# Performance work log

Hardware: AMD Instinct MI355X
Metric: run time of the kernel (lower is better)

Reference implementation:

```python
import jax, jax.numpy as jnp
import numpy as np

B, S, C = 16, 2048, 512
E = S            # embed_dim == seq_len (RMSNorm applied on transposed seq axis)
H = 4 * E        # FFN hidden
LAMBDA_INIT = float(0.8 - 0.6 * np.exp(-0.3 * 1.0))  # layer_index = 1
SCALE = E ** (-0.25)
K = 5            # decomposition moving-average kernel


def rmsnorm(x, w, eps=1e-8):
    return x * jax.lax.rsqrt(jnp.mean(x * x, axis=-1, keepdims=True) + eps) * w


def decompose(a):
    # DLinear-style series decomposition: replicate-padded moving average along seq
    pad = (K - 1) // 2
    ap = jnp.concatenate([jnp.repeat(a[:, :1], pad, axis=1), a, jnp.repeat(a[:, -1:], pad, axis=1)], axis=1)
    n = a.shape[1]
    trend = sum(ap[:, i:i + n] for i in range(K)) / K
    return trend, a - trend


def setup_inputs() -> dict:
    key = jax.random.key(0)
    ks = jax.random.split(key, 12)
    p = lambda i, shape, s=0.02: jax.random.normal(ks[i], shape, jnp.float32) * s
    return {
        "x": jax.random.normal(ks[0], (B, S, C), jnp.float32),
        "ln_attn_w": jnp.ones((E,), jnp.float32),
        "q12_w": p(1, (E, 2 * E)), "q12_b": jnp.zeros((2 * E,), jnp.float32),
        "k12_w": p(2, (E, 2 * E)), "k12_b": jnp.zeros((2 * E,), jnp.float32),
        "v_w": p(3, (E, E)), "v_b": jnp.zeros((E,), jnp.float32),
        "lambda_q1": p(4, (E,), 0.1), "lambda_k1": p(5, (E,), 0.1),
        "lambda_q2": p(6, (E,), 0.1), "lambda_k2": p(7, (E,), 0.1),
        "norm_w": jnp.ones((E,), jnp.float32),
        "ln_ff_w": jnp.ones((E,), jnp.float32),
        "ff_w1": p(8, (E, H)), "ff_b1": jnp.zeros((H,), jnp.float32),
        "ff_w2": p(9, (H, E)), "ff_b2": jnp.zeros((E,), jnp.float32),
    }


def reference(x, ln_attn_w, q12_w, q12_b, k12_w, k12_b, v_w, v_b,
              lambda_q1, lambda_k1, lambda_q2, lambda_k2,
              norm_w, ln_ff_w, ff_w1, ff_b1, ff_w2, ff_b2):
    # pre-attention RMSNorm over the seq axis (via transpose)
    a = jnp.swapaxes(rmsnorm(jnp.swapaxes(x, -1, -2), ln_attn_w), -1, -2)  # [B,S,C]
    trend, seasonal = decompose(a)
    # project seq dim of trend/seasonal (iTransformer style: channels are tokens)
    q = jnp.swapaxes(trend, -1, -2) @ q12_w + q12_b      # [B,C,2S]
    q1, q2 = jnp.split(q, 2, axis=-1)                    # [B,C,S] each
    k = jnp.swapaxes(seasonal, -1, -2) @ k12_w + k12_b   # [B,C,2S]
    k1, k2 = jnp.split(k, 2, axis=-1)                    # [B,C,S]
    v = jnp.swapaxes(a, -1, -2) @ v_w + v_b              # [B,C,S]
    a1 = jnp.einsum('bis,bjs->bij', q1, k1) * SCALE      # [B,C,C]
    a2 = jnp.einsum('bis,bjs->bij', q2, k2) * SCALE      # [B,C,C]
    lam = jnp.exp(jnp.sum(lambda_q1 * lambda_k1)) - jnp.exp(jnp.sum(lambda_q2 * lambda_k2)) + LAMBDA_INIT
    d = jax.nn.softmax(a1, axis=-1) - lam * jax.nn.softmax(a2, axis=-1)
    attn = rmsnorm(d @ v, norm_w) * (1.0 - LAMBDA_INIT)  # [B,C,S]
    x = x + jnp.swapaxes(attn, -1, -2)
    # FFN over the seq axis
    h = rmsnorm(jnp.swapaxes(x, -1, -2), ln_ff_w)        # [B,C,S]
    ff = jax.nn.gelu(h @ ff_w1 + ff_b1, approximate=False) @ ff_w2 + ff_b2
    return x + jnp.swapaxes(ff, -1, -2)
```

## Files before the change

kernel.cpp:

```cpp
#include <hip/hip_runtime.h>
#include <hip/hip_bf16.h>

#define B_ 16
#define S_ 2048
#define C_ 512
#define H_ 8192

#define LAMBDA_INIT_F 0.3555090675909693f
#define ONE_M_LI_F    0.6444909324090307f
#define SCALE_F       0.14865088937534013f

using bf16x8 = __attribute__((ext_vector_type(8))) short;
using f32x4  = __attribute__((ext_vector_type(4))) float;

__device__ __forceinline__ float b2f(ushort u) {
  union { unsigned u; float f; } x; x.u = ((unsigned)u) << 16; return x.f;
}
__device__ __forceinline__ ushort f2b(float f) {
  union { float f; unsigned u; } x; x.f = f;
  unsigned r = x.u + 0x7fffu + ((x.u >> 16) & 1u);
  return (ushort)(r >> 16);
}

__device__ __forceinline__ void load_lds16(const void* g, void* s) {
  __builtin_amdgcn_global_load_lds((const __attribute__((address_space(1))) void*)g,
                                   (__attribute__((address_space(3))) void*)s,
                                   16, 0, 0);
}

#define WAITV8() asm volatile("s_waitcnt vmcnt(8)" ::: "memory")
#define WAITV4() asm volatile("s_waitcnt vmcnt(4)" ::: "memory")
#define WAITV0() asm volatile("s_waitcnt vmcnt(0)" ::: "memory")
#define BARM()   asm volatile("s_barrier" ::: "memory")
#define BAR()    __builtin_amdgcn_s_barrier()

template <int EPI>
__global__ __launch_bounds__(512, 1) void gemm256(
    const ushort* __restrict__ A, const ushort* __restrict__ Bt,
    ushort* __restrict__ C, const float* __restrict__ bias,
    const ushort* __restrict__ addm,
    int K, int lda, int ldb, int ldc)
{
  __shared__ ushort lds[65536];
  const int t = threadIdx.x, w = t >> 6, lane = t & 63;
  const int fr = lane & 15, khl = lane >> 4;
  const int wr = w >> 2, wc = w & 3;

  const int gx = gridDim.x, gy = gridDim.y;
  const int id = blockIdx.y * gx + blockIdx.x;
  const int xcd = id & 7, l = id >> 3;
  const int tnb = (gy == 16) ? 3 : 2;
  const int lm = l >> tnb, ln = l & ((1 << tnb) - 1);
  const int m0 = ((xcd & 3) * 8 + lm) * 256;
  const int n0 = ((xcd >> 2) * (1 << tnb) + ln) * 256;

  const int sl    = (t & 7) ^ ((t >> 3) & 7);
  const int rbase = ((t >> 3) << 1) + (sl >> 2);
  const int khs   = sl & 3;
  const size_t aoff = (size_t)(m0 + rbase) * lda + khs * 8;
  const size_t boff = (size_t)(n0 + rbase) * ldb + khs * 8;
  const size_t jstA = (size_t)128 * lda, jstB = (size_t)128 * ldb;

  int ao[8], bo[4];
#pragma unroll
  for (int m = 0; m < 8; ++m) {
    const int row = wr * 128 + m * 16 + fr, dr = row >> 1;
    const int so = (((row & 1) << 2) + khl) ^ (dr & 7);
    ao[m] = dr * 64 + so * 8;
  }
#pragma unroll
  for (int n = 0; n < 4; ++n) {
    const int row = wc * 64 + n * 16 + fr, dr = row >> 1;
    const int so = (((row & 1) << 2) + khl) ^ (dr & 7);
    bo[n] = 8192 + dr * 64 + so * 8;
  }

  f32x4 acc[8][4] = {};
  const int U = K >> 5;

#define STAGE_U(u) do { \
    const ushort* sa_ = A  + aoff + (size_t)(u) * 32; \
    const ushort* sb_ = Bt + boff + (size_t)(u) * 32; \
    ushort* da_ = &lds[((u) & 3) * 16384 + w * 512]; \
    load_lds16(sa_, da_); load_lds16(sa_ + jstA, da_ + 4096); \
    load_lds16(sb_, da_ + 8192); load_lds16(sb_ + jstB, da_ + 12288); } while (0)
#define LDFRAG(u) do { const int sb_ = ((u) & 3) * 16384; \
    _Pragma("unroll") for (int m_ = 0; m_ < 8; ++m_) af[m_] = *(const bf16x8*)&lds[sb_ + ao[m_]]; \
    _Pragma("unroll") for (int n_ = 0; n_ < 4; ++n_) bg[n_] = *(const bf16x8*)&lds[sb_ + bo[n_]]; } while (0)
#define MFMA32() do { __builtin_amdgcn_s_setprio(1); \
    _Pragma("unroll") for (int m_ = 0; m_ < 8; ++m_) \
    _Pragma("unroll") for (int n_ = 0; n_ < 4; ++n_) \
      acc[m_][n_] = __builtin_amdgcn_mfma_f32_16x16x32_bf16(af[m_], bg[n_], acc[m_][n_], 0, 0, 0); \
    __builtin_amdgcn_s_setprio(0); } while (0)

  STAGE_U(0); STAGE_U(1); STAGE_U(2);
  WAITV8(); BARM();

  bf16x8 af[8], bg[4];
#pragma unroll 4
  for (int u = 0; u <= U - 4; ++u) {
    LDFRAG(u);
    STAGE_U(u + 3);
    MFMA32();
    WAITV8();
    BARM();
  }
  {
    LDFRAG(U - 3);
    MFMA32();
    WAITV4();
    BARM();
  }
  {
    LDFRAG(U - 2);
    MFMA32();
    WAITV0();
    BARM();
  }
  {
    LDFRAG(U - 1);
    MFMA32();
  }
#undef STAGE_U
#undef LDFRAG
#undef MFMA32

  const int r0 = khl * 4;
#pragma unroll
  for (int m = 0; m < 8; ++m)
#pragma unroll
    for (int nf = 0; nf < 4; ++nf) {
      const int gr = m0 + wr * 128 + m * 16 + r0;
      const int gc = n0 + wc * 64 + nf * 16 + fr;
      const float bb = (EPI == 3) ? 0.f : bias[gc];
#pragma unroll
      for (int r = 0; r < 4; ++r) {
        const size_t idx = (size_t)(gr + r) * ldc + gc;
        float v = acc[m][nf][r];
        if constexpr (EPI == 1) v += bb;
        if constexpr (EPI == 2) { v += bb; v = 0.5f * v * (1.f + erff(v * 0.7071067811865475f)); }
        if constexpr (EPI == 4) v += bb + b2f(addm[idx]) + b2f(C[idx]);
        C[idx] = f2b(v);
      }
    }
}

template <int EPI>
__global__ __launch_bounds__(256, 2) void gemm_nt(
    const ushort* __restrict__ Aall, const ushort* __restrict__ Ball,
    void* __restrict__ Call, int K, int lda, int ldb, int ldc,
    long sA, long sB, long sC, long sA2, long sB2, float alpha,
    const float* __restrict__ bias)
{
  __shared__ ushort lA[4096];
  __shared__ ushort lB[4096];
  const int t = threadIdx.x;
  const int m0 = blockIdx.x * 128, n0 = blockIdx.y * 128;
  const int zb = blockIdx.z & 15, zh = blockIdx.z >> 4;
  const ushort* A  = Aall + (size_t)zb * sA + (size_t)zh * sA2;
  const ushort* Bt = Ball + (size_t)zb * sB + (size_t)zh * sB2;
  const int lane = t & 63;
  const int wave = t >> 6;
  const int wm = (wave >> 1) * 64, wn = (wave & 1) * 64;
  const int fr = lane & 15, kh = lane >> 4;
  f32x4 acc[4][4] = {};
  const int srow = t >> 2;
  const int scol = (t & 3) * 8;
  const size_t ar0 = (size_t)(m0 + srow) * lda + scol;
  const size_t ar1 = (size_t)(m0 + 64 + srow) * lda + scol;
  const size_t br0 = (size_t)(n0 + srow) * ldb + scol;
  const size_t br1 = (size_t)(n0 + 64 + srow) * ldb + scol;
  const int wbase = wave * 512;

  for (int k0 = 0; k0 < K; k0 += 32) {
    __syncthreads();
    load_lds16(A + ar0 + k0,  &lA[wbase]);
    load_lds16(A + ar1 + k0,  &lA[2048 + wbase]);
    load_lds16(Bt + br0 + k0, &lB[wbase]);
    load_lds16(Bt + br1 + k0, &lB[2048 + wbase]);
    __syncthreads();
    bf16x8 af[4], bg[4];
#pragma unroll
    for (int i = 0; i < 4; ++i)
      af[i] = *(const bf16x8*)&lA[(wm + i * 16 + fr) * 32 + kh * 8];
#pragma unroll
    for (int j = 0; j < 4; ++j)
      bg[j] = *(const bf16x8*)&lB[(wn + j * 16 + fr) * 32 + kh * 8];
#pragma unroll
    for (int i = 0; i < 4; ++i)
#pragma unroll
      for (int j = 0; j < 4; ++j)
        acc[i][j] = __builtin_amdgcn_mfma_f32_16x16x32_bf16(af[i], bg[j], acc[i][j], 0, 0, 0);
  }

  const int r0 = kh * 4;
  if constexpr (EPI == 0) {
    float* C = (float*)Call + (size_t)blockIdx.z * sC;
#pragma unroll
    for (int i = 0; i < 4; ++i)
#pragma unroll
      for (int j = 0; j < 4; ++j) {
        const int gr = m0 + wm + i * 16 + r0;
        const int gc = n0 + wn + j * 16 + fr;
#pragma unroll
        for (int r = 0; r < 4; ++r)
          C[(size_t)(gr + r) * ldc + gc] = acc[i][j][r] * alpha;
      }
  } else {
    ushort* C = (ushort*)Call + (size_t)blockIdx.z * sC;
#pragma unroll
    for (int i = 0; i < 4; ++i)
#pragma unroll
      for (int j = 0; j < 4; ++j) {
        const int gr = m0 + wm + i * 16 + r0;
        const int gc = n0 + wn + j * 16 + fr;
#pragma unroll
        for (int r = 0; r < 4; ++r) {
          float v = acc[i][j][r];
          if constexpr (EPI == 3) v *= alpha;
          if constexpr (EPI == 5) v += bias[gr + r];
          C[(size_t)(gr + r) * ldc + gc] = f2b(v);
        }
      }
  }
}

__device__ __forceinline__ float block_sum(float v, float* red) {
#pragma unroll
  for (int o = 32; o > 0; o >>= 1) v += __shfl_down(v, o, 64);
  __syncthreads();
  if ((threadIdx.x & 63) == 0) red[threadIdx.x >> 6] = v;
  __syncthreads();
  return red[0] + red[1] + red[2] + red[3];
}
__device__ __forceinline__ float block_max(float v, float* red) {
#pragma unroll
  for (int o = 32; o > 0; o >>= 1) v = fmaxf(v, __shfl_down(v, o, 64));
  __syncthreads();
  if ((threadIdx.x & 63) == 0) red[threadIdx.x >> 6] = v;
  __syncthreads();
  return fmaxf(fmaxf(red[0], red[1]), fmaxf(red[2], red[3]));
}

__global__ __launch_bounds__(256) void k_rms_part(const float* __restrict__ x, float* __restrict__ part) {
  const int c = blockIdx.x * 256 + threadIdx.x;
  const int sl = blockIdx.y;
  const int b = blockIdx.z;
  const float* p = x + (size_t)b * S_ * C_ + c;
  const int s0 = sl * 256;
  float s = 0.f;
  for (int i = 0; i < 256; ++i) { float v = p[(size_t)(s0 + i) * C_]; s += v * v; }
  part[((size_t)b * C_ + c) * 8 + sl] = s;
}
__global__ __launch_bounds__(256) void k_rms_fin(const float* __restrict__ part, float* __restrict__ rms1) {
  const int i = blockIdx.x * 256 + threadIdx.x;
  const float* p = part + (size_t)i * 8;
  float s = 0.f;
#pragma unroll
  for (int j = 0; j < 8; ++j) s += p[j];
  rms1[i] = rsqrtf(s * (1.f / S_) + 1e-8f);
}

__global__ __launch_bounds__(256) void k_trans_norm(const float* __restrict__ x, const float* __restrict__ rms1,
                                                    const float* __restrict__ w,
                                                    ushort* __restrict__ aT, ushort* __restrict__ xT) {
  __shared__ float tile[32][33];
  const int s0 = blockIdx.x * 32, c0 = blockIdx.y * 32, b = blockIdx.z;
  const int tx = threadIdx.x, ty = threadIdx.y;
  const float* xb = x + (size_t)b * S_ * C_;
#pragma unroll
  for (int r = 0; r < 4; ++r) {
    const int s = ty + 8 * r;
    tile[s][tx] = xb[(size_t)(s0 + s) * C_ + c0 + tx];
  }
  __syncthreads();
#pragma unroll
  for (int r = 0; r < 4; ++r) {
    const int c = ty + 8 * r;
    const float v = tile[tx][c];
    const float rm = rms1[b * C_ + c0 + c];
    const size_t o = ((size_t)b * C_ + c0 + c) * S_ + s0 + tx;
    xT[o] = f2b(v);
    aT[o] = f2b(v * rm * w[s0 + tx]);
  }
}

__global__ __launch_bounds__(256) void k_wtrans(const float* __restrict__ W, ushort* __restrict__ WT,
                                                int Kd, int Ndstride, int n_base) {
  __shared__ float tile[32][33];
  const int k0 = blockIdx.x * 32, n0 = blockIdx.y * 32;
  const int tx = threadIdx.x, ty = threadIdx.y;
#pragma unroll
  for (int r = 0; r < 4; ++r) {
    const int k = ty + 8 * r;
    tile[k][tx] = W[(size_t)(k0 + k) * Ndstride + n_base + n0 + tx];
  }
  __syncthreads();
#pragma unroll
  for (int r = 0; r < 4; ++r) {
    const int n = ty + 8 * r;
    WT[(size_t)(n0 + n) * Kd + k0 + tx] = f2b(tile[tx][n]);
  }
}

__global__ __launch_bounds__(256) void k_convert(const float* __restrict__ in, ushort* __restrict__ out) {
  const size_t i = ((size_t)blockIdx.x * 256 + threadIdx.x) * 8;
  const f32x4 v0 = *(const f32x4*)(in + i);
  const f32x4 v1 = *(const f32x4*)(in + i + 4);
  bf16x8 o;
#pragma unroll
  for (int j = 0; j < 4; ++j) { o[j] = (short)f2b(v0[j]); o[4 + j] = (short)f2b(v1[j]); }
  *(bf16x8*)(out + i) = o;
}

__global__ __launch_bounds__(256) void k_matvec(const float* __restrict__ kw, const float* __restrict__ qb,
                                                float* __restrict__ vv) {
  __shared__ float red[4];
  const int s = blockIdx.x;
  const float* row = kw + (size_t)s * 4096;
  const int t = threadIdx.x;
  float s1 = 0.f, s2 = 0.f;
  for (int i = t; i < 2048; i += 256) { s1 += row[i] * qb[i]; s2 += row[2048 + i] * qb[2048 + i]; }
  s1 = block_sum(s1, red);
  s2 = block_sum(s2, red);
  if (t == 0) { vv[s] = s1; vv[2048 + s] = s2; }
}

__global__ __launch_bounds__(256) void k_gemv(const ushort* __restrict__ seT, const float* __restrict__ vv,
                                              float* __restrict__ rvec) {
  __shared__ float red[4];
  const int r = blockIdx.x;
  const ushort* row = seT + (size_t)r * 2048;
  const int t = threadIdx.x;
  float s1 = 0.f, s2 = 0.f;
  for (int i = t; i < 2048; i += 256) {
    const float sv = b2f(row[i]);
    s1 += sv * vv[i]; s2 += sv * vv[2048 + i];
  }
  s1 = block_sum(s1, red);
  s2 = block_sum(s2, red);
  if (t == 0) { rvec[r] = SCALE_F * s1; rvec[8192 + r] = SCALE_F * s2; }
}

__device__ __forceinline__ float trend5(const ushort* p, int s) {
  float sum = 0.f;
#pragma unroll
  for (int d = -2; d <= 2; ++d) {
    int ss = s + d; ss = ss < 0 ? 0 : (ss > S_ - 1 ? S_ - 1 : ss);
    sum += b2f(p[ss]);
  }
  return sum * 0.2f;
}
__global__ __launch_bounds__(256) void k_decomp2(const ushort* __restrict__ aT,
                                                 ushort* __restrict__ trT, ushort* __restrict__ seT) {
  const size_t i = (size_t)blockIdx.x * 256 + threadIdx.x;
  const int s = (int)(i & (S_ - 1));
  const ushort* p = aT + (i - s);
  const float tr = trend5(p, s);
  trT[i] = f2b(tr);
  seT[i] = f2b(b2f(p[s]) - tr);
}

__global__ __launch_bounds__(256) void k_lambda(const float* __restrict__ lq1, const float* __restrict__ lk1,
                                                const float* __restrict__ lq2, const float* __restrict__ lk2,
                                                float* __restrict__ lam) {
  __shared__ float r1[4], r2[4];
  const int t = threadIdx.x;
  float s1 = 0.f, s2 = 0.f;
  for (int i = t; i < S_; i += 256) { s1 += lq1[i] * lk1[i]; s2 += lq2[i] * lk2[i]; }
#pragma unroll
  for (int o = 32; o > 0; o >>= 1) { s1 += __shfl_down(s1, o, 64); s2 += __shfl_down(s2, o, 64); }
  if ((t & 63) == 0) { r1[t >> 6] = s1; r2[t >> 6] = s2; }
  __syncthreads();
  if (t == 0) {
    const float a = r1[0] + r1[1] + r1[2] + r1[3];
    const float b = r2[0] + r2[1] + r2[2] + r2[3];
    *lam = expf(a) - expf(b) + LAMBDA_INIT_F;
  }
}

__global__ __launch_bounds__(256) void k_softmax(const float* __restrict__ a1, const float* __restrict__ a2,
                                                 const float* __restrict__ lamp, const float* __restrict__ rvec,
                                                 ushort* __restrict__ dm) {
  __shared__ float red[4];
  const size_t row = blockIdx.x;
  const int jb = ((int)row >> 9) << 9;
  const float* p1 = a1 + row * 512;
  const float* p2 = a2 + row * 512;
  const int t = threadIdx.x;
  const float v1a = p1[t] + rvec[jb + t],        v1b = p1[t + 256] + rvec[jb + t + 256];
  const float v2a = p2[t] + rvec[8192 + jb + t], v2b = p2[t + 256] + rvec[8192 + jb + t + 256];
  const float m1 = block_max(fmaxf(v1a, v1b), red);
  const float m2 = block_max(fmaxf(v2a, v2b), red);
  const float e1a = expf(v1a - m1), e1b = expf(v1b - m1);
  const float e2a = expf(v2a - m2), e2b = expf(v2b - m2);
  const float s1 = block_sum(e1a + e1b, red);
  const float s2 = block_sum(e2a + e2b, red);
  const float i1 = 1.f / s1, i2 = (*lamp) / s2;
  ushort* o = dm + row * 512;
  o[t]       = f2b(e1a * i1 - e2a * i2);
  o[t + 256] = f2b(e1b * i1 - e2b * i2);
}

__global__ __launch_bounds__(256) void k_postattn(const ushort* __restrict__ P, const ushort* __restrict__ xT,
                                                  const float* __restrict__ norm_w, const float* __restrict__ ln_ff_w,
                                                  ushort* __restrict__ attn, ushort* __restrict__ h) {
  __shared__ float red[4];
  const size_t row = blockIdx.x;
  const ushort* p = P + row * S_;
  const int t = threadIdx.x;
  float v[8]; float ss = 0.f;
#pragma unroll
  for (int i = 0; i < 8; ++i) { v[i] = b2f(p[t + 256 * i]); ss += v[i] * v[i]; }
  ss = block_sum(ss, red);
  const float inv = rsqrtf(ss * (1.f / S_) + 1e-8f);
  const ushort* xr = xT + row * S_;
  ushort* ar = attn + row * S_;
  float x2[8]; float ss2 = 0.f;
#pragma unroll
  for (int i = 0; i < 8; ++i) {
    const int s = t + 256 * i;
    const float at = v[i] * inv * norm_w[s] * ONE_M_LI_F;
    ar[s] = f2b(at);
    const float xx = b2f(xr[s]) + at;
    x2[i] = xx; ss2 += xx * xx;
  }
  ss2 = block_sum(ss2, red);
  const float inv2 = rsqrtf(ss2 * (1.f / S_) + 1e-8f);
  ushort* hr = h + row * S_;
#pragma unroll
  for (int i = 0; i < 8; ++i) { const int s = t + 256 * i; hr[s] = f2b(x2[i] * inv2 * ln_ff_w[s]); }
}

__global__ __launch_bounds__(256) void k_final2(const float* __restrict__ x, const ushort* __restrict__ sumT,
                                                float* __restrict__ out) {
  __shared__ float tile[32][33];
  const int s0 = blockIdx.x * 32, c0 = blockIdx.y * 32, b = blockIdx.z;
  const int tx = threadIdx.x, ty = threadIdx.y;
#pragma unroll
  for (int r = 0; r < 4; ++r) {
    const int c = ty + 8 * r;
    tile[c][tx] = b2f(sumT[((size_t)b * C_ + c0 + c) * S_ + s0 + tx]);
  }
  __syncthreads();
#pragma unroll
  for (int r = 0; r < 4; ++r) {
    const int s = ty + 8 * r;
    const size_t o = ((size_t)b * S_ + s0 + s) * C_ + c0 + tx;
    out[o] = x[o] + tile[tx][s];
  }
}

__global__ void k_probe(float* out, float v) { out[0] = v; }

extern "C" void kernel_launch(void* const* d_in, const int* in_sizes, int n_in,
                              void* d_out, int out_size, void* d_ws, size_t ws_size,
                              hipStream_t stream) {
  const float* x       = (const float*)d_in[0];
  const float* ln_attn = (const float*)d_in[1];
  const float* q12_w   = (const float*)d_in[2];
  const float* q12_b   = (const float*)d_in[3];
  const float* k12_w   = (const float*)d_in[4];
  const float* k12_b   = (const float*)d_in[5];
  const float* v_w     = (const float*)d_in[6];
  const float* v_b     = (const float*)d_in[7];
  const float* lq1     = (const float*)d_in[8];
  const float* lk1     = (const float*)d_in[9];
  const float* lq2     = (const float*)d_in[10];
  const float* lk2     = (const float*)d_in[11];
  const float* norm_w  = (const float*)d_in[12];
  const float* ln_ff   = (const float*)d_in[13];
  const float* ff_w1   = (const float*)d_in[14];
  const float* ff_b1   = (const float*)d_in[15];
  const float* ff_w2   = (const float*)d_in[16];
  const float* ff_b2   = (const float*)d_in[17];
  float* out = (float*)d_out;

  if (ws_size < 184844544ull) {
    k_probe<<<1, 1, 0, stream>>>(out, (float)(ws_size >> 20));
    return;
  }

  char* ws = (char*)d_ws;
  ushort* slotA = (ushort*)(ws + 0);
  ushort* slotB = (ushort*)(ws + 33554432);
  ushort* slotC = (ushort*)(ws + 67108864);
  ushort* slotD = (ushort*)(ws + 100663296);
  ushort* slotE = (ushort*)(ws + 134217728);
  ushort* slotF = (ushort*)(ws + 167772160);
  float*  part  = (float*) (ws + 184549376);
  float*  rms1  = (float*) (ws + 184811520);
  float*  lamp  = (float*) (ws + 184844288);

  ushort* aT   = slotA;
  ushort* k12c = slotA;
  ushort* T12s = slotA;
  ushort* hbuf = slotA;
  ushort* trT  = slotB;
  ushort* Pm   = slotB;
  ushort* ff1T = slotB;
  ushort* seT  = slotC;
  ushort* attn = slotC;
  ushort* VT   = slotD;
  ushort* ff2T = slotD;
  ushort* xT   = slotE;
  ushort* ffo  = slotE;
  ushort* wsl  = slotF;
  ushort* q12c = slotF;
  ushort* dmat = slotF;
  float*  vvb  = (float*)(ws + 167772160 + 12582912);
  float*  rvec = vvb + 4096;
  ushort* M12T = (ushort*)d_out;
  float*  scr  = (float*)((char*)d_out + 16777216);
  ushort* H1   = (ushort*)d_out;

  const dim3 blk256(256), blk512(512), blkT(32, 8);

  k_rms_part<<<dim3(2, 8, B_), blk256, 0, stream>>>(x, part);
  k_rms_fin<<<dim3(32), blk256, 0, stream>>>(part, rms1);
  k_trans_norm<<<dim3(64, 16, B_), blkT, 0, stream>>>(x, rms1, ln_attn, aT, xT);

  k_wtrans<<<dim3(64, 64), blkT, 0, stream>>>(v_w, wsl, 2048, 2048, 0);
  gemm_nt<5><<<dim3(16, 4, 16), blk256, 0, stream>>>(wsl, aT, VT, 2048, 2048, 2048, 512,
                                                     0, 1048576, 1048576, 0, 0, 1.f, v_b);

  k_decomp2<<<dim3(65536), blk256, 0, stream>>>(aT, trT, seT);
  k_lambda<<<dim3(1), blk256, 0, stream>>>(lq1, lk1, lq2, lk2, lamp);

  k_convert<<<dim3(4096), blk256, 0, stream>>>(q12_w, q12c);
  k_convert<<<dim3(4096), blk256, 0, stream>>>(k12_w, k12c);
  gemm_nt<3><<<dim3(16, 16, 2), blk256, 0, stream>>>(k12c, q12c, M12T, 2048, 4096, 4096, 2048,
                                                     2048, 2048, 4194304, 0, 0, 1.f, nullptr);

  k_matvec<<<dim3(2048), blk256, 0, stream>>>(k12_w, q12_b, vvb);
  k_gemv<<<dim3(8192), blk256, 0, stream>>>(seT, vvb, rvec);

  gemm256<3><<<dim3(32, 8), blk512, 0, stream>>>(trT, M12T, T12s, nullptr, nullptr,
                                                 2048, 2048, 2048, 2048);
  gemm_nt<0><<<dim3(4, 4, 16), blk256, 0, stream>>>(T12s, seT, scr, 2048, 2048, 2048, 512,
                                                    1048576, 1048576, 262144, 0, 0, SCALE_F, nullptr);
  gemm256<3><<<dim3(32, 8), blk512, 0, stream>>>(trT, M12T + 4194304, T12s, nullptr, nullptr,
                                                 2048, 2048, 2048, 2048);
  gemm_nt<0><<<dim3(4, 4, 16), blk256, 0, stream>>>(T12s, seT, scr + 4194304, 2048, 2048, 2048, 512,
                                                    1048576, 1048576, 262144, 0, 0, SCALE_F, nullptr);

  k_softmax<<<dim3(8192), blk256, 0, stream>>>(scr, scr + 4194304, lamp, rvec, dmat);
  gemm_nt<3><<<dim3(4, 16, B_), blk256, 0, stream>>>(dmat, VT, Pm, 512, 512, 512, 2048,
                                                     262144, 1048576, 1048576, 0, 0, 1.f, nullptr);

  k_postattn<<<dim3(8192), blk256, 0, stream>>>(Pm, xT, norm_w, ln_ff, attn, hbuf);

  k_wtrans<<<dim3(64, 256), blkT, 0, stream>>>(ff_w1, ff1T, 2048, 8192, 0);
  k_wtrans<<<dim3(256, 64), blkT, 0, stream>>>(ff_w2, ff2T, 8192, 2048, 0);

  gemm256<2><<<dim3(32, 16), blk512, 0, stream>>>(hbuf, ff1T, H1, ff_b1, nullptr,
                                                  2048, 2048, 2048, 4096);
  gemm256<3><<<dim3(32, 8), blk512, 0, stream>>>(H1, ff2T, ffo, nullptr, nullptr,
                                                 4096, 4096, 8192, 2048);
  gemm256<2><<<dim3(32, 16), blk512, 0, stream>>>(hbuf, ff1T + (size_t)4096 * 2048, H1,
                                                  ff_b1 + 4096, nullptr, 2048, 2048, 2048, 4096);
  gemm256<4><<<dim3(32, 8), blk512, 0, stream>>>(H1, ff2T + 4096, ffo, ff_b2, attn,
                                                 4096, 4096, 8192, 2048);

  k_final2<<<dim3(64, 16, B_), blkT, 0, stream>>>(x, ffo, out);
}
```

Baseline: 1.183 ms.

## Shrink gemm256 tile to 256x128 with triple-buffered LDS for higher occupancy

The 256x256 GEMM tile is cut to 256x128, with 8 waves arranged 4x2, each computing 64x64. The LDS ring goes from four stages to three, and a larger occupancy target is declared through launch_bounds. Grids are doubled along N to match. The aim is more resident blocks per CU and fewer accumulator registers, so latency hides better and the grid fills the GPU more evenly. The cost is less data reuse per tile, which means more global and LDS traffic per FLOP, and a shallower prefetch pipeline.

```diff
diff --git a/kernel.cpp b/kernel.cpp
--- a/kernel.cpp
+++ b/kernel.cpp
@@ -28,43 +28,41 @@
                                    16, 0, 0);
 }
 
-#define WAITV8() asm volatile("s_waitcnt vmcnt(8)" ::: "memory")
-#define WAITV4() asm volatile("s_waitcnt vmcnt(4)" ::: "memory")
+#define WAITV3() asm volatile("s_waitcnt vmcnt(3)" ::: "memory")
 #define WAITV0() asm volatile("s_waitcnt vmcnt(0)" ::: "memory")
 #define BARM()   asm volatile("s_barrier" ::: "memory")
-#define BAR()    __builtin_amdgcn_s_barrier()
 
 template <int EPI>
-__global__ __launch_bounds__(512, 1) void gemm256(
+__global__ __launch_bounds__(512, 4) void gemm256(
     const ushort* __restrict__ A, const ushort* __restrict__ Bt,
     ushort* __restrict__ C, const float* __restrict__ bias,
     const ushort* __restrict__ addm,
     int K, int lda, int ldb, int ldc)
 {
-  __shared__ ushort lds[65536];
+  __shared__ ushort lds[36864];
   const int t = threadIdx.x, w = t >> 6, lane = t & 63;
   const int fr = lane & 15, khl = lane >> 4;
-  const int wr = w >> 2, wc = w & 3;
+  const int wr = w >> 1, wc = w & 1;
 
   const int gx = gridDim.x, gy = gridDim.y;
   const int id = blockIdx.y * gx + blockIdx.x;
   const int xcd = id & 7, l = id >> 3;
-  const int tnb = (gy == 16) ? 3 : 2;
+  const int tnb = (gy == 32) ? 4 : 3;
   const int lm = l >> tnb, ln = l & ((1 << tnb) - 1);
   const int m0 = ((xcd & 3) * 8 + lm) * 256;
-  const int n0 = ((xcd >> 2) * (1 << tnb) + ln) * 256;
+  const int n0 = ((xcd >> 2) * (1 << tnb) + ln) * 128;
 
   const int sl    = (t & 7) ^ ((t >> 3) & 7);
   const int rbase = ((t >> 3) << 1) + (sl >> 2);
   const int khs   = sl & 3;
   const size_t aoff = (size_t)(m0 + rbase) * lda + khs * 8;
   const size_t boff = (size_t)(n0 + rbase) * ldb + khs * 8;
-  const size_t jstA = (size_t)128 * lda, jstB = (size_t)128 * ldb;
-
-  int ao[8], bo[4];
-#pragma unroll
-  for (int m = 0; m < 8; ++m) {
-    const int row = wr * 128 + m * 16 + fr, dr = row >> 1;
+  const size_t jstA = (size_t)128 * lda;
+
+  int ao[4], bo[4];
+#pragma unroll
+  for (int m = 0; m < 4; ++m) {
+    const int row = wr * 64 + m * 16 + fr, dr = row >> 1;
     const int so = (((row & 1) << 2) + khl) ^ (dr & 7);
     ao[m] = dr * 64 + so * 8;
   }
@@ -75,62 +73,63 @@
     bo[n] = 8192 + dr * 64 + so * 8;
   }
 
-  f32x4 acc[8][4] = {};
+  f32x4 acc[4][4] = {};
   const int U = K >> 5;
 
-#define STAGE_U(u) do { \
+#define STAGE_U(u, slot) do { \
     const ushort* sa_ = A  + aoff + (size_t)(u) * 32; \
     const ushort* sb_ = Bt + boff + (size_t)(u) * 32; \
-    ushort* da_ = &lds[((u) & 3) * 16384 + w * 512]; \
+    ushort* da_ = &lds[(slot) + w * 512]; \
     load_lds16(sa_, da_); load_lds16(sa_ + jstA, da_ + 4096); \
-    load_lds16(sb_, da_ + 8192); load_lds16(sb_ + jstB, da_ + 12288); } while (0)
-#define LDFRAG(u) do { const int sb_ = ((u) & 3) * 16384; \
-    _Pragma("unroll") for (int m_ = 0; m_ < 8; ++m_) af[m_] = *(const bf16x8*)&lds[sb_ + ao[m_]]; \
-    _Pragma("unroll") for (int n_ = 0; n_ < 4; ++n_) bg[n_] = *(const bf16x8*)&lds[sb_ + bo[n_]]; } while (0)
-#define MFMA32() do { __builtin_amdgcn_s_setprio(1); \
-    _Pragma("unroll") for (int m_ = 0; m_ < 8; ++m_) \
+    load_lds16(sb_, da_ + 8192); } while (0)
+#define LDFRAG(slot) do { \
+    _Pragma("unroll") for (int m_ = 0; m_ < 4; ++m_) af[m_] = *(const bf16x8*)&lds[(slot) + ao[m_]]; \
+    _Pragma("unroll") for (int n_ = 0; n_ < 4; ++n_) bg[n_] = *(const bf16x8*)&lds[(slot) + bo[n_]]; } while (0)
+#define MFMA16() do { __builtin_amdgcn_s_setprio(1); \
+    _Pragma("unroll") for (int m_ = 0; m_ < 4; ++m_) \
     _Pragma("unroll") for (int n_ = 0; n_ < 4; ++n_) \
       acc[m_][n_] = __builtin_amdgcn_mfma_f32_16x16x32_bf16(af[m_], bg[n_], acc[m_][n_], 0, 0, 0); \
     __builtin_amdgcn_s_setprio(0); } while (0)
 
-  STAGE_U(0); STAGE_U(1); STAGE_U(2);
-  WAITV8(); BARM();
-
-  bf16x8 af[8], bg[4];
-#pragma unroll 4
-  for (int u = 0; u <= U - 4; ++u) {
-    LDFRAG(u);
-    STAGE_U(u + 3);
-    MFMA32();
-    WAITV8();
+  STAGE_U(0, 0); STAGE_U(1, 12288);
+  WAITV3(); BARM();
+
+  bf16x8 af[4], bg[4];
+  int cur = 0, stg = 24576;
+#pragma unroll 3
+  for (int u = 0; u <= U - 3; ++u) {
+    LDFRAG(cur);
+    STAGE_U(u + 2, stg);
+    MFMA16();
+    WAITV3();
     BARM();
+    const int nx = cur + 12288;
+    cur = (nx == 36864) ? 0 : nx;
+    const int ns = stg + 12288;
+    stg = (ns == 36864) ? 0 : ns;
   }
   {
-    LDFRAG(U - 3);
-    MFMA32();
-    WAITV4();
-    BARM();
-  }
-  {
-    LDFRAG(U - 2);
-    MFMA32();
+    LDFRAG(cur);
+    MFMA16();
     WAITV0();
     BARM();
+    const int nx = cur + 12288;
+    cur = (nx == 36864) ? 0 : nx;
   }
   {
-    LDFRAG(U - 1);
-    MFMA32();
+    LDFRAG(cur);
+    MFMA16();
   }
 #undef STAGE_U
 #undef LDFRAG
-#undef MFMA32
+#undef MFMA16
 
   const int r0 = khl * 4;
 #pragma unroll
-  for (int m = 0; m < 8; ++m)
+  for (int m = 0; m < 4; ++m)
 #pragma unroll
     for (int nf = 0; nf < 4; ++nf) {
-      const int gr = m0 + wr * 128 + m * 16 + r0;
+      const int gr = m0 + wr * 64 + m * 16 + r0;
       const int gc = n0 + wc * 64 + nf * 16 + fr;
       const float bb = (EPI == 3) ? 0.f : bias[gc];
 #pragma unroll
@@ -535,12 +534,12 @@
   k_matvec<<<dim3(2048), blk256, 0, stream>>>(k12_w, q12_b, vvb);
   k_gemv<<<dim3(8192), blk256, 0, stream>>>(seT, vvb, rvec);
 
-  gemm256<3><<<dim3(32, 8), blk512, 0, stream>>>(trT, M12T, T12s, nullptr, nullptr,
-                                                 2048, 2048, 2048, 2048);
+  gemm256<3><<<dim3(32, 16), blk512, 0, stream>>>(trT, M12T, T12s, nullptr, nullptr,
+                                                  2048, 2048, 2048, 2048);
   gemm_nt<0><<<dim3(4, 4, 16), blk256, 0, stream>>>(T12s, seT, scr, 2048, 2048, 2048, 512,
                                                     1048576, 1048576, 262144, 0, 0, SCALE_F, nullptr);
-  gemm256<3><<<dim3(32, 8), blk512, 0, stream>>>(trT, M12T + 4194304, T12s, nullptr, nullptr,
-                                                 2048, 2048, 2048, 2048);
+  gemm256<3><<<dim3(32, 16), blk512, 0, stream>>>(trT, M12T + 4194304, T12s, nullptr, nullptr,
+                                                  2048, 2048, 2048, 2048);
   gemm_nt<0><<<dim3(4, 4, 16), blk256, 0, stream>>>(T12s, seT, scr + 4194304, 2048, 2048, 2048, 512,
                                                     1048576, 1048576, 262144, 0, 0, SCALE_F, nullptr);
 
@@ -553,14 +552,14 @@
   k_wtrans<<<dim3(64, 256), blkT, 0, stream>>>(ff_w1, ff1T, 2048, 8192, 0);
   k_wtrans<<<dim3(256, 64), blkT, 0, stream>>>(ff_w2, ff2T, 8192, 2048, 0);
 
-  gemm256<2><<<dim3(32, 16), blk512, 0, stream>>>(hbuf, ff1T, H1, ff_b1, nullptr,
+  gemm256<2><<<dim3(32, 32), blk512, 0, stream>>>(hbuf, ff1T, H1, ff_b1, nullptr,
                                                   2048, 2048, 2048, 4096);
-  gemm256<3><<<dim3(32, 8), blk512, 0, stream>>>(H1, ff2T, ffo, nullptr, nullptr,
-                                                 4096, 4096, 8192, 2048);
-  gemm256<2><<<dim3(32, 16), blk512, 0, stream>>>(hbuf, ff1T + (size_t)4096 * 2048, H1,
+  gemm256<3><<<dim3(32, 16), blk512, 0, stream>>>(H1, ff2T, ffo, nullptr, nullptr,
+                                                  4096, 4096, 8192, 2048);
+  gemm256<2><<<dim3(32, 32), blk512, 0, stream>>>(hbuf, ff1T + (size_t)4096 * 2048, H1,
                                                   ff_b1 + 4096, nullptr, 2048, 2048, 2048, 4096);
-  gemm256<4><<<dim3(32, 8), blk512, 0, stream>>>(H1, ff2T + 4096, ffo, ff_b2, attn,
-                                                 4096, 4096, 8192, 2048);
+  gemm256<4><<<dim3(32, 16), blk512, 0, stream>>>(H1, ff2T + 4096, ffo, ff_b2, attn,
+                                                  4096, 4096, 8192, 2048);
 
   k_final2<<<dim3(64, 16, B_), blkT, 0, stream>>>(x, ffo, out);
 }
```

Result: no change. 1.191 ms (+0.7%).
